# Optimization experiments

Measured on AMD Instinct MI355X. Metric: run time of the kernel, lower is better.

Reference implementation:

```python
import jax, jax.numpy as jnp
import numpy as np

B, T, D = 2, 2048, 1024
H = 16
HD = D // H  # 64

def setup_inputs() -> dict:
    key = jax.random.key(0)
    k1, k2, k3 = jax.random.split(key, 3)
    x = jax.random.normal(k1, (B, T, D), dtype=jnp.float32)
    # Linear weights stored as [in, out] for x @ W (torch stores [out, in])
    W_qkv = jax.random.normal(k2, (D, 3 * D), dtype=jnp.float32) * (1.0 / np.sqrt(D))
    W_proj = jax.random.normal(k3, (D, D), dtype=jnp.float32) * (1.0 / np.sqrt(D))
    return {"x": x, "W_qkv": W_qkv, "W_proj": W_proj}

def reference(x, W_qkv, W_proj):
    Bx, Tx, C = x.shape
    qkv = x @ W_qkv                             # [B, T, 3D]
    q, k, v = jnp.split(qkv, 3, axis=-1)        # each [B, T, D]
    # [B, T, H, HD] -> [B, H, T, HD]
    q = q.reshape(Bx, Tx, H, HD).transpose(0, 2, 1, 3)
    k = k.reshape(Bx, Tx, H, HD).transpose(0, 2, 1, 3)
    v = v.reshape(Bx, Tx, H, HD).transpose(0, 2, 1, 3)
    scale = 1.0 / np.sqrt(HD).astype(np.float32)
    att = jnp.einsum('bhqd,bhkd->bhqk', q, k) * scale  # [B, H, T, T]
    causal = jnp.tril(jnp.ones((Tx, Tx), dtype=bool))
    att = jnp.where(causal[None, None, :, :], att, -jnp.inf)
    att = jax.nn.softmax(att, axis=-1)
    y = jnp.einsum('bhqk,bhkd->bhqd', att, v)   # [B, H, T, HD]
    y = y.transpose(0, 2, 1, 3).reshape(Bx, Tx, C)
    return y @ W_proj
```

## Files before the change

### kernel.cpp

```cpp
#include <hip/hip_runtime.h>

typedef __bf16 bf16x8 __attribute__((ext_vector_type(8)));
typedef __bf16 bf16x4 __attribute__((ext_vector_type(4)));
typedef float f32x4 __attribute__((ext_vector_type(4)));
typedef unsigned short u16;
typedef unsigned int u32;
typedef u32 u32x4 __attribute__((ext_vector_type(4)));

__device__ __forceinline__ u16 f2bf(float f) {
  u32 u = __builtin_bit_cast(u32, f);
  u += 0x7fffu + ((u >> 16) & 1u);
  return (u16)(u >> 16);
}

__device__ __forceinline__ u32 cvt_pk_bf16(float lo, float hi) {
  u32 r;
  asm("v_cvt_pk_bf16_f32 %0, %1, %2" : "=v"(r) : "v"(lo), "v"(hi));
  return r;
}

__device__ __forceinline__ float ex2(float x) {
  float r;
  asm("v_exp_f32 %0, %1" : "=v"(r) : "v"(x));
  return r;
}

__device__ __forceinline__ void gl_lds16(const u16* g, u16* l) {
  __builtin_amdgcn_global_load_lds(
      (const __attribute__((address_space(1))) u32*)g,
      (__attribute__((address_space(3))) u32*)l, 16, 0, 0);
}

__device__ __forceinline__ bf16x4 tr16(const u16* p) {
  bf16x4 r;
  auto lp = (const __attribute__((address_space(3))) u16*)p;
  asm volatile("ds_read_b64_tr_b16 %0, %1" : "=&v"(r) : "v"(lp));
  return r;
}

__global__ __launch_bounds__(256) void k_cast(const float* __restrict__ in,
                                              u16* __restrict__ out, int n8) {
  int i = blockIdx.x * 256 + threadIdx.x;
  if (i >= n8) return;
  const float4* p = (const float4*)in + (size_t)i * 2;
  float4 a = p[0], b = p[1];
  u16 r[8] = {f2bf(a.x), f2bf(a.y), f2bf(a.z), f2bf(a.w),
              f2bf(b.x), f2bf(b.y), f2bf(b.z), f2bf(b.w)};
  ((uint4*)out)[i] = *(const uint4*)r;
}

__global__ __launch_bounds__(256) void k_tcast(const float* __restrict__ in,
                                               u16* __restrict__ out, int K, int N) {
  __shared__ float tile[32][33];
  int n0 = blockIdx.x * 32, k0 = blockIdx.y * 32;
  int c = threadIdx.x & 31, r0 = (threadIdx.x >> 5) * 4;
#pragma unroll
  for (int rr = 0; rr < 4; ++rr) {
    int r = r0 + rr;
    tile[r][c] = in[(size_t)(k0 + r) * N + n0 + c];
  }
  __syncthreads();
#pragma unroll
  for (int rr = 0; rr < 4; ++rr) {
    int r = r0 + rr;
    out[(size_t)(n0 + r) * K + k0 + c] = f2bf(tile[c][r]);
  }
}

template <int EPI>
__global__ __launch_bounds__(256) void k_gemm(const u16* __restrict__ A,
                                              const u16* __restrict__ Bt,
                                              u16* __restrict__ Qp, u16* __restrict__ Kp,
                                              u16* __restrict__ Vp, float* __restrict__ Cf,
                                              int K) {
  __shared__ char smem[128 * 136 * 2];
  u16* As = (u16*)smem;
  u16* Bs = (u16*)(smem + 16384);
  u16* Cs = (u16*)smem;
  const int tid = threadIdx.x;
  const int lane = tid & 63, wave = tid >> 6;
  const int l15 = lane & 15, l4 = lane >> 4;
  const int wr = wave >> 1, wc = wave & 1;
  const int tm = blockIdx.y, tn = blockIdx.x;

  int srow[4], scol[4];
#pragma unroll
  for (int i = 0; i < 4; ++i) {
    srow[i] = wave * 32 + i * 8 + (lane >> 3);
    scol[i] = ((lane & 7) ^ (srow[i] & 7)) * 8;
  }

  const f32x4 fz = {0.f, 0.f, 0.f, 0.f};
  f32x4 acc[4][4];
#pragma unroll
  for (int a = 0; a < 4; ++a)
#pragma unroll
    for (int b = 0; b < 4; ++b) acc[a][b] = fz;

  const int nk = K >> 6;
  for (int kt = 0; kt < nk; ++kt) {
#pragma unroll
    for (int i = 0; i < 4; ++i)
      gl_lds16(A + (size_t)(tm * 128 + srow[i]) * K + kt * 64 + scol[i],
               &As[(wave * 4 + i) * 512]);
#pragma unroll
    for (int i = 0; i < 4; ++i)
      gl_lds16(Bt + (size_t)(tn * 128 + srow[i]) * K + kt * 64 + scol[i],
               &Bs[(wave * 4 + i) * 512]);
    __syncthreads();
    bf16x8 af[2][4], bfr[2][4];
#pragma unroll
    for (int s = 0; s < 2; ++s) {
#pragma unroll
      for (int mi = 0; mi < 4; ++mi) {
        int row = wr * 64 + mi * 16 + l15;
        int pch = (s * 4 + l4) ^ (row & 7);
        af[s][mi] = *(const bf16x8*)&As[row * 64 + pch * 8];
      }
#pragma unroll
      for (int ni = 0; ni < 4; ++ni) {
        int row = wc * 64 + ni * 16 + l15;
        int pch = (s * 4 + l4) ^ (row & 7);
        bfr[s][ni] = *(const bf16x8*)&Bs[row * 64 + pch * 8];
      }
    }
    __builtin_amdgcn_s_setprio(1);
#pragma unroll
    for (int s = 0; s < 2; ++s)
#pragma unroll
      for (int mi = 0; mi < 4; ++mi)
#pragma unroll
        for (int ni = 0; ni < 4; ++ni)
          acc[mi][ni] = __builtin_amdgcn_mfma_f32_16x16x32_bf16(af[s][mi], bfr[s][ni],
                                                                acc[mi][ni], 0, 0, 0);
    __builtin_amdgcn_s_setprio(0);
    __syncthreads();
  }

  if (EPI == 0) {
#pragma unroll
    for (int ni = 0; ni < 4; ++ni) {
      int colb = wc * 64 + ni * 16;
      float scl = ((tn * 128 + colb) >> 10) == 0 ? 0.180336880f : 1.0f;
#pragma unroll
      for (int mi = 0; mi < 4; ++mi)
#pragma unroll
        for (int r = 0; r < 4; ++r) {
          int rowb = wr * 64 + mi * 16 + l4 * 4 + r;
          Cs[rowb * 136 + colb + l15] = f2bf(acc[mi][ni][r] * scl);
        }
    }
    __syncthreads();
#pragma unroll
    for (int pass = 0; pass < 8; ++pass) {
      int rowb = pass * 16 + (tid >> 4);
      int colb = (tid & 15) * 8;
      uint4 v = *(const uint4*)&Cs[rowb * 136 + colb];
      int rowg = tm * 128 + rowb;
      int b = rowg >> 11, t = rowg & 2047;
      int gcol = tn * 128 + colb;
      int which = gcol >> 10;
      int d = gcol & 1023;
      int h = d >> 6, hd = d & 63;
      u16* dst = which == 0 ? Qp : (which == 1 ? Kp : Vp);
      *(uint4*)&dst[(size_t)(((b * 16 + h) * 2048 + t) * 64 + hd)] = v;
    }
  } else {
    const int rbase = tm * 128 + wr * 64 + l4 * 4;
    const int cbase = tn * 128 + wc * 64 + l15;
#pragma unroll
    for (int mi = 0; mi < 4; ++mi)
#pragma unroll
      for (int r = 0; r < 4; ++r) {
        int rowg = rbase + mi * 16 + r;
#pragma unroll
        for (int ni = 0; ni < 4; ++ni)
          Cf[(size_t)rowg * 1024 + cbase + ni * 16] = acc[mi][ni][r];
      }
  }
}

__global__ __launch_bounds__(256) void k_attn(const u16* __restrict__ Q,
                                              const u16* __restrict__ K,
                                              const u16* __restrict__ V,
                                              u16* __restrict__ Y) {
  __shared__ u16 Kl[4][64 * 64];
  __shared__ u16 Vtr[4][64 * 64];
  const int tid = threadIdx.x, lane = tid & 63, wave = tid >> 6;
  const int l15 = lane & 15, l4 = lane >> 4;
  const int bh = blockIdx.y;
  const int pp = (blockIdx.x + ((blockIdx.y >> 4) << 3)) & 15;
  const int qtA = 31 - pp, qtB = pp;
  const u16* Qb = Q + (size_t)bh * 2048 * 64;
  const u16* Kb = K + (size_t)bh * 2048 * 64;
  const u16* Vb = V + (size_t)bh * 2048 * 64;
  const int b = bh >> 4, h = bh & 15;
  const f32x4 fz = {0.f, 0.f, 0.f, 0.f};

  const int kk0 = wave * 16 + (lane >> 3);
  const int kk1 = kk0 + 8;
  const int lcol0 = ((lane & 7) ^ (kk0 & 7)) * 8;
  const int lcol1 = ((lane & 7) ^ (kk1 & 7)) * 8;
  int vk[2], vhd[2];
#pragma unroll
  for (int i = 0; i < 2; ++i) {
    int o = (wave * 2 + i) * 512 + lane * 8;
    vk[i] = ((o >> 6) & 15) * 4 + ((o >> 4) & 3);
    vhd[i] = ((o >> 10) << 4) + (o & 8);
  }

  auto stage = [&](int buf, int kt) {
    gl_lds16(Kb + (size_t)(kt * 64 + kk0) * 64 + lcol0, &Kl[buf][(wave * 2 + 0) * 512]);
    gl_lds16(Kb + (size_t)(kt * 64 + kk1) * 64 + lcol1, &Kl[buf][(wave * 2 + 1) * 512]);
    gl_lds16(Vb + (size_t)(kt * 64 + vk[0]) * 64 + vhd[0], &Vtr[buf][(wave * 2 + 0) * 512]);
    gl_lds16(Vb + (size_t)(kt * 64 + vk[1]) * 64 + vhd[1], &Vtr[buf][(wave * 2 + 1) * 512]);
  };

  auto qk = [&](int buf, const bf16x8* qf, f32x4* accS) {
#pragma unroll
    for (int s = 0; s < 2; ++s)
#pragma unroll
      for (int nb = 0; nb < 4; ++nb) {
        int kk = nb * 16 + l15;
        int ch = (s * 4 + l4) ^ (kk & 7);
        bf16x8 kf = *(const bf16x8*)&Kl[buf][kk * 64 + ch * 8];
        accS[nb] = __builtin_amdgcn_mfma_f32_16x16x32_bf16(kf, qf[s], accS[nb], 0, 0, 0);
      }
  };
  auto pv = [&](int buf, const bf16x8* pf, f32x4* accO) {
#pragma unroll
    for (int s = 0; s < 2; ++s) {
      bf16x8 vf[4];
#pragma unroll
      for (int hb = 0; hb < 4; ++hb) {
        bf16x4 ta = tr16(&Vtr[buf][(hb * 16 + s * 8) * 64 + lane * 4]);
        bf16x4 tb = tr16(&Vtr[buf][(hb * 16 + s * 8 + 4) * 64 + lane * 4]);
        vf[hb] = __builtin_shufflevector(ta, tb, 0, 1, 2, 3, 4, 5, 6, 7);
      }
      asm volatile("s_waitcnt lgkmcnt(0)" ::: "memory");
      __builtin_amdgcn_sched_barrier(0);
      __builtin_amdgcn_s_setprio(1);
#pragma unroll
      for (int hb = 0; hb < 4; ++hb)
        accO[hb] = __builtin_amdgcn_mfma_f32_16x16x32_bf16(vf[hb], pf[s], accO[hb], 0, 0, 0);
      __builtin_amdgcn_s_setprio(0);
    }
  };

  bf16x8 qfA[2], qfB[2];
  {
    int qrA = qtA * 64 + wave * 16 + l15;
    int qrB = qtB * 64 + wave * 16 + l15;
    qfA[0] = *(const bf16x8*)&Qb[(size_t)qrA * 64 + l4 * 8];
    qfA[1] = *(const bf16x8*)&Qb[(size_t)qrA * 64 + 32 + l4 * 8];
    qfB[0] = *(const bf16x8*)&Qb[(size_t)qrB * 64 + l4 * 8];
    qfB[1] = *(const bf16x8*)&Qb[(size_t)qrB * 64 + 32 + l4 * 8];
  }
  f32x4 oA[4] = {fz, fz, fz, fz}, oB[4] = {fz, fz, fz, fz};
  float mA = -1e30f, lsA = 0.f, mB = -1e30f, lsB = 0.f;

  stage(0, 0);
  stage(1, 1);
  stage(2, 2);
  int cur = 0;
#pragma unroll 1
  for (int kt = 0; kt <= qtB; ++kt) {
    asm volatile("s_waitcnt vmcnt(8)" ::: "memory");
    __builtin_amdgcn_s_barrier();
    __builtin_amdgcn_sched_barrier(0);

    f32x4 sA[4] = {fz, fz, fz, fz}, sB[4] = {fz, fz, fz, fz};
    __builtin_amdgcn_s_setprio(1);
#pragma unroll
    for (int s = 0; s < 2; ++s)
#pragma unroll
      for (int nb = 0; nb < 4; ++nb) {
        int kk = nb * 16 + l15;
        int ch = (s * 4 + l4) ^ (kk & 7);
        bf16x8 kf = *(const bf16x8*)&Kl[cur][kk * 64 + ch * 8];
        sA[nb] = __builtin_amdgcn_mfma_f32_16x16x32_bf16(kf, qfA[s], sA[nb], 0, 0, 0);
        sB[nb] = __builtin_amdgcn_mfma_f32_16x16x32_bf16(kf, qfB[s], sB[nb], 0, 0, 0);
      }
    __builtin_amdgcn_s_setprio(0);

    float vA[16], vB[16];
#pragma unroll
    for (int nb = 0; nb < 4; ++nb)
#pragma unroll
      for (int r = 0; r < 4; ++r) {
        vA[nb * 4 + r] = sA[nb][r];
        vB[nb * 4 + r] = sB[nb][r];
      }
    if (kt == qtB) {
      int qg = wave * 16 + l15;
#pragma unroll
      for (int i = 0; i < 16; ++i) {
        int kg = (i >> 2) * 16 + l4 * 4 + (i & 3);
        if (kg > qg) vB[i] = -1e30f;
      }
    }
    float tA[8], tB[8];
#pragma unroll
    for (int i = 0; i < 8; ++i) {
      tA[i] = fmaxf(vA[2 * i], vA[2 * i + 1]);
      tB[i] = fmaxf(vB[2 * i], vB[2 * i + 1]);
    }
#pragma unroll
    for (int i = 0; i < 4; ++i) {
      tA[i] = fmaxf(tA[i], tA[i + 4]);
      tB[i] = fmaxf(tB[i], tB[i + 4]);
    }
    float mxA = fmaxf(fmaxf(tA[0], tA[2]), fmaxf(tA[1], tA[3]));
    float mxB = fmaxf(fmaxf(tB[0], tB[2]), fmaxf(tB[1], tB[3]));
    if (!__all(fmaxf(mxA - mA, mxB - mB) <= 8.0f)) {
      float mrA = fmaxf(mxA, __shfl_xor(mxA, 16));
      float mrB = fmaxf(mxB, __shfl_xor(mxB, 16));
      mrA = fmaxf(mrA, __shfl_xor(mrA, 32));
      mrB = fmaxf(mrB, __shfl_xor(mrB, 32));
      float mnA = fmaxf(mA, mrA), mnB = fmaxf(mB, mrB);
      float aA = ex2(mA - mnA), aB = ex2(mB - mnB);
      mA = mnA;
      mB = mnB;
      lsA *= aA;
      lsB *= aB;
#pragma unroll
      for (int hb = 0; hb < 4; ++hb)
#pragma unroll
        for (int r = 0; r < 4; ++r) {
          oA[hb][r] *= aA;
          oB[hb][r] *= aB;
        }
    }
    float pA[16], pB[16];
#pragma unroll
    for (int i = 0; i < 16; ++i) {
      pA[i] = ex2(vA[i] - mA);
      pB[i] = ex2(vB[i] - mB);
    }
    float uA[8], uB[8];
#pragma unroll
    for (int i = 0; i < 8; ++i) {
      uA[i] = pA[2 * i] + pA[2 * i + 1];
      uB[i] = pB[2 * i] + pB[2 * i + 1];
    }
#pragma unroll
    for (int i = 0; i < 4; ++i) {
      uA[i] += uA[i + 4];
      uB[i] += uB[i + 4];
    }
    lsA += (uA[0] + uA[2]) + (uA[1] + uA[3]);
    lsB += (uB[0] + uB[2]) + (uB[1] + uB[3]);
    bf16x8 pfA[2], pfB[2];
#pragma unroll
    for (int s = 0; s < 2; ++s) {
      u32x4 wa, wb;
      wa.x = cvt_pk_bf16(pA[8 * s + 0], pA[8 * s + 1]);
      wb.x = cvt_pk_bf16(pB[8 * s + 0], pB[8 * s + 1]);
      wa.y = cvt_pk_bf16(pA[8 * s + 2], pA[8 * s + 3]);
      wb.y = cvt_pk_bf16(pB[8 * s + 2], pB[8 * s + 3]);
      wa.z = cvt_pk_bf16(pA[8 * s + 4], pA[8 * s + 5]);
      wb.z = cvt_pk_bf16(pB[8 * s + 4], pB[8 * s + 5]);
      wa.w = cvt_pk_bf16(pA[8 * s + 6], pA[8 * s + 7]);
      wb.w = cvt_pk_bf16(pB[8 * s + 6], pB[8 * s + 7]);
      pfA[s] = __builtin_bit_cast(bf16x8, wa);
      pfB[s] = __builtin_bit_cast(bf16x8, wb);
    }
#pragma unroll
    for (int s = 0; s < 2; ++s) {
      bf16x8 vf[4];
#pragma unroll
      for (int hb = 0; hb < 4; ++hb) {
        bf16x4 ta = tr16(&Vtr[cur][(hb * 16 + s * 8) * 64 + lane * 4]);
        bf16x4 tb = tr16(&Vtr[cur][(hb * 16 + s * 8 + 4) * 64 + lane * 4]);
        vf[hb] = __builtin_shufflevector(ta, tb, 0, 1, 2, 3, 4, 5, 6, 7);
      }
      asm volatile("s_waitcnt lgkmcnt(0)" ::: "memory");
      __builtin_amdgcn_sched_barrier(0);
      __builtin_amdgcn_s_setprio(1);
#pragma unroll
      for (int hb = 0; hb < 4; ++hb) {
        oA[hb] = __builtin_amdgcn_mfma_f32_16x16x32_bf16(vf[hb], pfA[s], oA[hb], 0, 0, 0);
        oB[hb] = __builtin_amdgcn_mfma_f32_16x16x32_bf16(vf[hb], pfB[s], oB[hb], 0, 0, 0);
      }
      __builtin_amdgcn_s_setprio(0);
    }

    int nt = kt + 3 > qtB ? qtB : kt + 3;
    stage((cur + 3) & 3, nt);
    cur = (cur + 1) & 3;
  }

  const int t0 = qtB + 1;
  const int rem = qtA - qtB;
  const int nd = (rem - 1) >> 1;
  __builtin_amdgcn_s_barrier();
  __builtin_amdgcn_sched_barrier(0);
#pragma unroll
  for (int i = 0; i < 4; ++i) {
    int tt = t0 + i > qtA ? qtA : t0 + i;
    stage(i, tt);
  }

  auto smx2 = [&](f32x4* s1, f32x4* s2, bf16x8* pf1, bf16x8* pf2) {
    float v1[16], v2[16];
#pragma unroll
    for (int nb = 0; nb < 4; ++nb)
#pragma unroll
      for (int r = 0; r < 4; ++r) {
        v1[nb * 4 + r] = s1[nb][r];
        v2[nb * 4 + r] = s2[nb][r];
      }
    float t1[8], t2[8];
#pragma unroll
    for (int i = 0; i < 8; ++i) {
      t1[i] = fmaxf(v1[2 * i], v1[2 * i + 1]);
      t2[i] = fmaxf(v2[2 * i], v2[2 * i + 1]);
    }
#pragma unroll
    for (int i = 0; i < 4; ++i) {
      t1[i] = fmaxf(t1[i], t1[i + 4]);
      t2[i] = fmaxf(t2[i], t2[i + 4]);
    }
    float mx = fmaxf(fmaxf(fmaxf(t1[0], t1[2]), fmaxf(t1[1], t1[3])),
                     fmaxf(fmaxf(t2[0], t2[2]), fmaxf(t2[1], t2[3])));
    if (!__all(mx <= mA + 8.0f)) {
      float mr = fmaxf(mx, __shfl_xor(mx, 16));
      mr = fmaxf(mr, __shfl_xor(mr, 32));
      float mn = fmaxf(mA, mr);
      float a = ex2(mA - mn);
      mA = mn;
      lsA *= a;
#pragma unroll
      for (int hb = 0; hb < 4; ++hb)
#pragma unroll
        for (int r = 0; r < 4; ++r) oA[hb][r] *= a;
    }
    float p1[16], p2[16];
#pragma unroll
    for (int i = 0; i < 16; ++i) {
      p1[i] = ex2(v1[i] - mA);
      p2[i] = ex2(v2[i] - mA);
    }
    float u1[8], u2[8];
#pragma unroll
    for (int i = 0; i < 8; ++i) {
      u1[i] = p1[2 * i] + p1[2 * i + 1];
      u2[i] = p2[2 * i] + p2[2 * i + 1];
    }
#pragma unroll
    for (int i = 0; i < 4; ++i) {
      u1[i] += u1[i + 4];
      u2[i] += u2[i + 4];
    }
    lsA += (u1[0] + u1[2]) + (u1[1] + u1[3]) + (u2[0] + u2[2]) + (u2[1] + u2[3]);
#pragma unroll
    for (int s = 0; s < 2; ++s) {
      u32x4 w1, w2;
      w1.x = cvt_pk_bf16(p1[8 * s + 0], p1[8 * s + 1]);
      w2.x = cvt_pk_bf16(p2[8 * s + 0], p2[8 * s + 1]);
      w1.y = cvt_pk_bf16(p1[8 * s + 2], p1[8 * s + 3]);
      w2.y = cvt_pk_bf16(p2[8 * s + 2], p2[8 * s + 3]);
      w1.z = cvt_pk_bf16(p1[8 * s + 4], p1[8 * s + 5]);
      w2.z = cvt_pk_bf16(p2[8 * s + 4], p2[8 * s + 5]);
      w1.w = cvt_pk_bf16(p1[8 * s + 6], p1[8 * s + 7]);
      w2.w = cvt_pk_bf16(p2[8 * s + 6], p2[8 * s + 7]);
      pf1[s] = __builtin_bit_cast(bf16x8, w1);
      pf2[s] = __builtin_bit_cast(bf16x8, w2);
    }
  };

#pragma unroll 1
  for (int j = 0; j < nd; ++j) {
    asm volatile("s_waitcnt vmcnt(8)" ::: "memory");
    __builtin_amdgcn_s_barrier();
    __builtin_amdgcn_sched_barrier(0);
    int b0 = (2 * j) & 3, b1 = (2 * j + 1) & 3;

    f32x4 s1[4] = {fz, fz, fz, fz}, s2[4] = {fz, fz, fz, fz};
    __builtin_amdgcn_s_setprio(1);
    qk(b0, qfA, s1);
    qk(b1, qfA, s2);
    __builtin_amdgcn_s_setprio(0);
    bf16x8 pf1[2], pf2[2];
    smx2(s1, s2, pf1, pf2);
    pv(b0, pf1, oA);
    pv(b1, pf2, oA);

    __builtin_amdgcn_s_barrier();
    __builtin_amdgcn_sched_barrier(0);
    int ta = t0 + 2 * j + 4, tb2 = t0 + 2 * j + 5;
    stage(b0, ta > qtA ? qtA : ta);
    stage(b1, tb2 > qtA ? qtA : tb2);
  }

  {
    asm volatile("s_waitcnt vmcnt(8)" ::: "memory");
    __builtin_amdgcn_s_barrier();
    __builtin_amdgcn_sched_barrier(0);
    int buf = (rem - 1) & 3;
    f32x4 sA[4] = {fz, fz, fz, fz};
    __builtin_amdgcn_s_setprio(1);
    qk(buf, qfA, sA);
    __builtin_amdgcn_s_setprio(0);
    float vA[16];
#pragma unroll
    for (int nb = 0; nb < 4; ++nb)
#pragma unroll
      for (int r = 0; r < 4; ++r) vA[nb * 4 + r] = sA[nb][r];
    int qg = wave * 16 + l15;
#pragma unroll
    for (int i = 0; i < 16; ++i) {
      int kg = (i >> 2) * 16 + l4 * 4 + (i & 3);
      if (kg > qg) vA[i] = -1e30f;
    }
    float tA[8];
#pragma unroll
    for (int i = 0; i < 8; ++i) tA[i] = fmaxf(vA[2 * i], vA[2 * i + 1]);
#pragma unroll
    for (int i = 0; i < 4; ++i) tA[i] = fmaxf(tA[i], tA[i + 4]);
    float mxA = fmaxf(fmaxf(tA[0], tA[2]), fmaxf(tA[1], tA[3]));
    if (!__all(mxA <= mA + 8.0f)) {
      float mrA = fmaxf(mxA, __shfl_xor(mxA, 16));
      mrA = fmaxf(mrA, __shfl_xor(mrA, 32));
      float mnA = fmaxf(mA, mrA);
      float aA = ex2(mA - mnA);
      mA = mnA;
      lsA *= aA;
#pragma unroll
      for (int hb = 0; hb < 4; ++hb)
#pragma unroll
        for (int r = 0; r < 4; ++r) oA[hb][r] *= aA;
    }
    float pA[16];
#pragma unroll
    for (int i = 0; i < 16; ++i) pA[i] = ex2(vA[i] - mA);
    float uA[8];
#pragma unroll
    for (int i = 0; i < 8; ++i) uA[i] = pA[2 * i] + pA[2 * i + 1];
#pragma unroll
    for (int i = 0; i < 4; ++i) uA[i] += uA[i + 4];
    lsA += (uA[0] + uA[2]) + (uA[1] + uA[3]);
    bf16x8 pfA[2];
#pragma unroll
    for (int s = 0; s < 2; ++s) {
      u32x4 wa;
      wa.x = cvt_pk_bf16(pA[8 * s + 0], pA[8 * s + 1]);
      wa.y = cvt_pk_bf16(pA[8 * s + 2], pA[8 * s + 3]);
      wa.z = cvt_pk_bf16(pA[8 * s + 4], pA[8 * s + 5]);
      wa.w = cvt_pk_bf16(pA[8 * s + 6], pA[8 * s + 7]);
      pfA[s] = __builtin_bit_cast(bf16x8, wa);
    }
    pv(buf, pfA, oA);
  }

  auto epi = [&](f32x4* accO, float lsum, int qt) {
    float t = lsum + __shfl_xor(lsum, 16);
    t += __shfl_xor(t, 32);
    float inv = 1.0f / t;
    int qg = qt * 64 + wave * 16 + l15;
    u16* yrow = Y + (size_t)(b * 2048 + qg) * 1024 + h * 64;
#pragma unroll
    for (int hb = 0; hb < 4; ++hb) {
      uint2 pk;
      pk.x = cvt_pk_bf16(accO[hb][0] * inv, accO[hb][1] * inv);
      pk.y = cvt_pk_bf16(accO[hb][2] * inv, accO[hb][3] * inv);
      *(uint2*)&yrow[hb * 16 + l4 * 4] = pk;
    }
  };
  epi(oA, lsA, qtA);
  epi(oB, lsB, qtB);
}

extern "C" void kernel_launch(void* const* d_in, const int* in_sizes, int n_in,
                              void* d_out, int out_size, void* d_ws, size_t ws_size,
                              hipStream_t stream) {
  const float* x = (const float*)d_in[0];
  const float* Wqkv = (const float*)d_in[1];
  const float* Wproj = (const float*)d_in[2];
  float* out = (float*)d_out;

  char* ws = (char*)d_ws;
  u16* Xb  = (u16*)(ws + 0);
  u16* Wqt = (u16*)(ws + ((size_t)8 << 20));
  u16* Wpt = (u16*)(ws + ((size_t)14 << 20));
  u16* Qs  = (u16*)(ws + ((size_t)16 << 20));
  u16* Ks  = (u16*)(ws + ((size_t)24 << 20));
  u16* Vs  = (u16*)(ws + ((size_t)32 << 20));
  u16* Yb  = (u16*)(ws + ((size_t)40 << 20));

  k_cast<<<2048, 256, 0, stream>>>(x, Xb, 4096 * 1024 / 8);
  k_tcast<<<dim3(96, 32), 256, 0, stream>>>(Wqkv, Wqt, 1024, 3072);
  k_tcast<<<dim3(32, 32), 256, 0, stream>>>(Wproj, Wpt, 1024, 1024);
  k_gemm<0><<<dim3(24, 32), 256, 0, stream>>>(Xb, Wqt, Qs, Ks, Vs, nullptr, 1024);
  k_attn<<<dim3(16, 32), 256, 0, stream>>>(Qs, Ks, Vs, Yb);
  k_gemm<1><<<dim3(8, 32), 256, 0, stream>>>(Yb, Wpt, nullptr, nullptr, nullptr, out, 1024);
}
```

Before: 106.8 us.

## Replace QKV GEMM with 256x256-tile, 512-thread, triple-buffered direct-to-LDS kernel

Adds a new QKV projection kernel that computes 256x256 output tiles with 8 waves. It loads operands straight into LDS through the gl_lds16 path, using a three-stage ring buffer with a partial vmcnt wait so loads overlap the MFMA work. The goal is more data reuse per tile and better hiding of global-load latency than the old 128x128 kernel. The trade-off is a grid of only 192 blocks on a GPU with many CUs, which can leave some CUs idle, plus heavy register use for 32 accumulators per wave. The output projection becomes a non-templated copy of the old kernel.

```diff
diff --git a/kernel.cpp b/kernel.cpp
--- a/kernel.cpp
+++ b/kernel.cpp
@@ -67,16 +67,112 @@
   }
 }
 
-template <int EPI>
-__global__ __launch_bounds__(256) void k_gemm(const u16* __restrict__ A,
+__global__ __launch_bounds__(512) void k_g256(const u16* __restrict__ A,
                                               const u16* __restrict__ Bt,
                                               u16* __restrict__ Qp, u16* __restrict__ Kp,
-                                              u16* __restrict__ Vp, float* __restrict__ Cf,
-                                              int K) {
-  __shared__ char smem[128 * 136 * 2];
-  u16* As = (u16*)smem;
-  u16* Bs = (u16*)(smem + 16384);
-  u16* Cs = (u16*)smem;
+                                              u16* __restrict__ Vp) {
+  __shared__ u16 lds[65536];
+  const int tid = threadIdx.x, lane = tid & 63, wave = tid >> 6;
+  const int l15 = lane & 15, l4 = lane >> 4;
+  const int wm = wave >> 2, wn = wave & 3;
+  const int tn = blockIdx.x, tm = blockIdx.y;
+
+  int srow[2], scg[2];
+#pragma unroll
+  for (int j = 0; j < 2; ++j) {
+    int o16 = j * 512 + tid;
+    srow[j] = o16 >> 2;
+    scg[j] = (tid & 3) ^ (srow[j] & 3);
+  }
+  auto stage = [&](int buf, int kt) {
+#pragma unroll
+    for (int j = 0; j < 2; ++j)
+      gl_lds16(A + (size_t)(tm * 256 + srow[j]) * 1024 + kt * 32 + scg[j] * 8,
+               &lds[buf * 16384 + j * 4096 + wave * 512]);
+#pragma unroll
+    for (int j = 0; j < 2; ++j)
+      gl_lds16(Bt + (size_t)(tn * 256 + srow[j]) * 1024 + kt * 32 + scg[j] * 8,
+               &lds[buf * 16384 + 8192 + j * 4096 + wave * 512]);
+  };
+
+  const f32x4 fz = {0.f, 0.f, 0.f, 0.f};
+  f32x4 acc[8][4];
+#pragma unroll
+  for (int m = 0; m < 8; ++m)
+#pragma unroll
+    for (int n = 0; n < 4; ++n) acc[m][n] = fz;
+
+  const int crd = l4 ^ (l15 & 3);
+
+  stage(0, 0);
+  stage(1, 1);
+
+#pragma unroll 1
+  for (int g = 0; g < 32; ++g) {
+    const int cur = g % 3;
+    asm volatile("s_waitcnt vmcnt(4)" ::: "memory");
+    __builtin_amdgcn_s_barrier();
+    __builtin_amdgcn_sched_barrier(0);
+
+    bf16x8 af[8], bf[4];
+#pragma unroll
+    for (int m = 0; m < 8; ++m) {
+      int row = wm * 128 + m * 16 + l15;
+      af[m] = *(const bf16x8*)&lds[cur * 16384 + row * 32 + crd * 8];
+    }
+#pragma unroll
+    for (int n = 0; n < 4; ++n) {
+      int row = wn * 64 + n * 16 + l15;
+      bf[n] = *(const bf16x8*)&lds[cur * 16384 + 8192 + row * 32 + crd * 8];
+    }
+    int nt = g + 2 > 31 ? 31 : g + 2;
+    stage((g + 2) % 3, nt);
+
+    __builtin_amdgcn_s_setprio(1);
+#pragma unroll
+    for (int m = 0; m < 8; ++m)
+#pragma unroll
+      for (int n = 0; n < 4; ++n)
+        acc[m][n] = __builtin_amdgcn_mfma_f32_16x16x32_bf16(af[m], bf[n], acc[m][n], 0, 0, 0);
+    __builtin_amdgcn_s_setprio(0);
+  }
+
+  asm volatile("s_waitcnt vmcnt(0)" ::: "memory");
+  __builtin_amdgcn_s_barrier();
+  const float scl = (tn < 4) ? 0.180336880f : 1.0f;
+#pragma unroll
+  for (int m = 0; m < 8; ++m) {
+    int rowb = wm * 128 + m * 16 + l4 * 4;
+#pragma unroll
+    for (int n = 0; n < 4; ++n) {
+      int colb = wn * 64 + n * 16 + l15;
+#pragma unroll
+      for (int r = 0; r < 4; ++r)
+        lds[(rowb + r) * 256 + colb] = f2bf(acc[m][n][r] * scl);
+    }
+  }
+  __syncthreads();
+  const int which = tn >> 2;
+  u16* dst = which == 0 ? Qp : (which == 1 ? Kp : Vp);
+#pragma unroll
+  for (int pass = 0; pass < 16; ++pass) {
+    int rowb = pass * 16 + (tid >> 5);
+    int colb = (tid & 31) * 8;
+    uint4 v = *(const uint4*)&lds[rowb * 256 + colb];
+    int rowg = tm * 256 + rowb;
+    int b = rowg >> 11, t = rowg & 2047;
+    int gcol = tn * 256 + colb;
+    int d = gcol & 1023;
+    int h = d >> 6, hd = d & 63;
+    *(uint4*)&dst[(size_t)(((b * 16 + h) * 2048 + t) * 64 + hd)] = v;
+  }
+}
+
+__global__ __launch_bounds__(256) void k_gemm1(const u16* __restrict__ A,
+                                               const u16* __restrict__ Bt,
+                                               float* __restrict__ Cf, int K) {
+  __shared__ u16 As[128 * 64];
+  __shared__ u16 Bs[128 * 64];
   const int tid = threadIdx.x;
   const int lane = tid & 63, wave = tid >> 6;
   const int l15 = lane & 15, l4 = lane >> 4;
@@ -137,47 +233,17 @@
     __syncthreads();
   }
 
-  if (EPI == 0) {
-#pragma unroll
-    for (int ni = 0; ni < 4; ++ni) {
-      int colb = wc * 64 + ni * 16;
-      float scl = ((tn * 128 + colb) >> 10) == 0 ? 0.180336880f : 1.0f;
-#pragma unroll
-      for (int mi = 0; mi < 4; ++mi)
-#pragma unroll
-        for (int r = 0; r < 4; ++r) {
-          int rowb = wr * 64 + mi * 16 + l4 * 4 + r;
-          Cs[rowb * 136 + colb + l15] = f2bf(acc[mi][ni][r] * scl);
-        }
-    }
-    __syncthreads();
-#pragma unroll
-    for (int pass = 0; pass < 8; ++pass) {
-      int rowb = pass * 16 + (tid >> 4);
-      int colb = (tid & 15) * 8;
-      uint4 v = *(const uint4*)&Cs[rowb * 136 + colb];
-      int rowg = tm * 128 + rowb;
-      int b = rowg >> 11, t = rowg & 2047;
-      int gcol = tn * 128 + colb;
-      int which = gcol >> 10;
-      int d = gcol & 1023;
-      int h = d >> 6, hd = d & 63;
-      u16* dst = which == 0 ? Qp : (which == 1 ? Kp : Vp);
-      *(uint4*)&dst[(size_t)(((b * 16 + h) * 2048 + t) * 64 + hd)] = v;
-    }
-  } else {
-    const int rbase = tm * 128 + wr * 64 + l4 * 4;
-    const int cbase = tn * 128 + wc * 64 + l15;
-#pragma unroll
-    for (int mi = 0; mi < 4; ++mi)
-#pragma unroll
-      for (int r = 0; r < 4; ++r) {
-        int rowg = rbase + mi * 16 + r;
-#pragma unroll
-        for (int ni = 0; ni < 4; ++ni)
-          Cf[(size_t)rowg * 1024 + cbase + ni * 16] = acc[mi][ni][r];
-      }
-  }
+  const int rbase = tm * 128 + wr * 64 + l4 * 4;
+  const int cbase = tn * 128 + wc * 64 + l15;
+#pragma unroll
+  for (int mi = 0; mi < 4; ++mi)
+#pragma unroll
+    for (int r = 0; r < 4; ++r) {
+      int rowg = rbase + mi * 16 + r;
+#pragma unroll
+      for (int ni = 0; ni < 4; ++ni)
+        Cf[(size_t)rowg * 1024 + cbase + ni * 16] = acc[mi][ni][r];
+    }
 }
 
 __global__ __launch_bounds__(256) void k_attn(const u16* __restrict__ Q,
@@ -591,7 +657,7 @@
   k_cast<<<2048, 256, 0, stream>>>(x, Xb, 4096 * 1024 / 8);
   k_tcast<<<dim3(96, 32), 256, 0, stream>>>(Wqkv, Wqt, 1024, 3072);
   k_tcast<<<dim3(32, 32), 256, 0, stream>>>(Wproj, Wpt, 1024, 1024);
-  k_gemm<0><<<dim3(24, 32), 256, 0, stream>>>(Xb, Wqt, Qs, Ks, Vs, nullptr, 1024);
+  k_g256<<<dim3(12, 16), 512, 0, stream>>>(Xb, Wqt, Qs, Ks, Vs);
   k_attn<<<dim3(16, 32), 256, 0, stream>>>(Qs, Ks, Vs, Yb);
-  k_gemm<1><<<dim3(8, 32), 256, 0, stream>>>(Yb, Wpt, nullptr, nullptr, nullptr, out, 1024);
-}
+  k_gemm1<<<dim3(8, 32), 256, 0, stream>>>(Yb, Wpt, out, 1024);
+}
```

Result: slower. 113.8 us (+6.5%).

## Triple-buffer GEMM LDS staging with K=32 tiles and prefetch two ahead

Applied to the files above, without the earlier changes.

Restructures the bf16 GEMM main loop into a three-stage LDS ring buffer holding K=32 slices. Global-to-LDS loads for iteration kt+2 are issued while iteration kt computes, and a single barrier per iteration is gated by vmcnt, replacing the load, sync, compute, sync pattern. This is meant to hide global memory latency behind MFMA work. In exchange the swizzle is reduced to 4 chunks, LDS use grows to 48KB, there are twice as many iterations each doing half the MFMAs, and the last iterations issue redundant clamped loads.

```diff
diff --git a/kernel.cpp b/kernel.cpp
--- a/kernel.cpp
+++ b/kernel.cpp
@@ -73,22 +73,30 @@
                                               u16* __restrict__ Qp, u16* __restrict__ Kp,
                                               u16* __restrict__ Vp, float* __restrict__ Cf,
                                               int K) {
-  __shared__ char smem[128 * 136 * 2];
-  u16* As = (u16*)smem;
-  u16* Bs = (u16*)(smem + 16384);
-  u16* Cs = (u16*)smem;
+  __shared__ u16 lds[24576];
   const int tid = threadIdx.x;
   const int lane = tid & 63, wave = tid >> 6;
   const int l15 = lane & 15, l4 = lane >> 4;
   const int wr = wave >> 1, wc = wave & 1;
   const int tm = blockIdx.y, tn = blockIdx.x;
 
-  int srow[4], scol[4];
-#pragma unroll
-  for (int i = 0; i < 4; ++i) {
-    srow[i] = wave * 32 + i * 8 + (lane >> 3);
-    scol[i] = ((lane & 7) ^ (srow[i] & 7)) * 8;
-  }
+  int srow[2], scg[2];
+#pragma unroll
+  for (int j = 0; j < 2; ++j) {
+    int o16 = j * 256 + wave * 64 + lane;
+    srow[j] = o16 >> 2;
+    scg[j] = (lane & 3) ^ (srow[j] & 3);
+  }
+  auto stage = [&](int buf, int kt) {
+#pragma unroll
+    for (int j = 0; j < 2; ++j)
+      gl_lds16(A + (size_t)(tm * 128 + srow[j]) * K + kt * 32 + scg[j] * 8,
+               &lds[buf * 8192 + j * 2048 + wave * 512]);
+#pragma unroll
+    for (int j = 0; j < 2; ++j)
+      gl_lds16(Bt + (size_t)(tn * 128 + srow[j]) * K + kt * 32 + scg[j] * 8,
+               &lds[buf * 8192 + 4096 + j * 2048 + wave * 512]);
+  };
 
   const f32x4 fz = {0.f, 0.f, 0.f, 0.f};
   f32x4 acc[4][4];
@@ -97,47 +105,48 @@
 #pragma unroll
     for (int b = 0; b < 4; ++b) acc[a][b] = fz;
 
-  const int nk = K >> 6;
+  const int nk = K >> 5;
+  stage(0, 0);
+  stage(1, 1);
+
+#pragma unroll 1
   for (int kt = 0; kt < nk; ++kt) {
-#pragma unroll
-    for (int i = 0; i < 4; ++i)
-      gl_lds16(A + (size_t)(tm * 128 + srow[i]) * K + kt * 64 + scol[i],
-               &As[(wave * 4 + i) * 512]);
-#pragma unroll
-    for (int i = 0; i < 4; ++i)
-      gl_lds16(Bt + (size_t)(tn * 128 + srow[i]) * K + kt * 64 + scol[i],
-               &Bs[(wave * 4 + i) * 512]);
-    __syncthreads();
-    bf16x8 af[2][4], bfr[2][4];
-#pragma unroll
-    for (int s = 0; s < 2; ++s) {
-#pragma unroll
-      for (int mi = 0; mi < 4; ++mi) {
-        int row = wr * 64 + mi * 16 + l15;
-        int pch = (s * 4 + l4) ^ (row & 7);
-        af[s][mi] = *(const bf16x8*)&As[row * 64 + pch * 8];
-      }
-#pragma unroll
-      for (int ni = 0; ni < 4; ++ni) {
-        int row = wc * 64 + ni * 16 + l15;
-        int pch = (s * 4 + l4) ^ (row & 7);
-        bfr[s][ni] = *(const bf16x8*)&Bs[row * 64 + pch * 8];
-      }
-    }
+    asm volatile("s_waitcnt vmcnt(4)" ::: "memory");
+    __builtin_amdgcn_s_barrier();
+    __builtin_amdgcn_sched_barrier(0);
+    const int cur = kt % 3;
+
+    bf16x8 af[4], bfr[4];
+#pragma unroll
+    for (int mi = 0; mi < 4; ++mi) {
+      int row = wr * 64 + mi * 16 + l15;
+      int pch = l4 ^ (row & 3);
+      af[mi] = *(const bf16x8*)&lds[cur * 8192 + row * 32 + pch * 8];
+    }
+#pragma unroll
+    for (int ni = 0; ni < 4; ++ni) {
+      int row = wc * 64 + ni * 16 + l15;
+      int pch = l4 ^ (row & 3);
+      bfr[ni] = *(const bf16x8*)&lds[cur * 8192 + 4096 + row * 32 + pch * 8];
+    }
+    int nt = kt + 2 >= nk ? nk - 1 : kt + 2;
+    stage((kt + 2) % 3, nt);
+
     __builtin_amdgcn_s_setprio(1);
 #pragma unroll
-    for (int s = 0; s < 2; ++s)
-#pragma unroll
-      for (int mi = 0; mi < 4; ++mi)
-#pragma unroll
-        for (int ni = 0; ni < 4; ++ni)
-          acc[mi][ni] = __builtin_amdgcn_mfma_f32_16x16x32_bf16(af[s][mi], bfr[s][ni],
-                                                                acc[mi][ni], 0, 0, 0);
+    for (int mi = 0; mi < 4; ++mi)
+#pragma unroll
+      for (int ni = 0; ni < 4; ++ni)
+        acc[mi][ni] = __builtin_amdgcn_mfma_f32_16x16x32_bf16(af[mi], bfr[ni],
+                                                              acc[mi][ni], 0, 0, 0);
     __builtin_amdgcn_s_setprio(0);
-    __syncthreads();
-  }
+  }
+
+  asm volatile("s_waitcnt vmcnt(0)" ::: "memory");
+  __builtin_amdgcn_s_barrier();
 
   if (EPI == 0) {
+    u16* Cs = lds;
 #pragma unroll
     for (int ni = 0; ni < 4; ++ni) {
       int colb = wc * 64 + ni * 16;
```

Measured after the change: 108.0 us. No clear change (+1.1%).
